# Performance work log

Measured on AMD Instinct MI355X. Metric: run time of the kernel, lower is better.

## Reference

```python
import jax, jax.numpy as jnp
import numpy as np
from jax import lax

BATCH, SEQ = 2, 2048
D_MODEL, D_STATE, D_CONV, D_INNER, DT_RANK = 1024, 16, 4, 2048, 64


def setup_inputs() -> dict:
    key = jax.random.key(0)
    ks = jax.random.split(key, 8)
    n = lambda k, shape, scale: (jax.random.normal(k, shape, jnp.float32) * scale)
    A = jnp.tile(jnp.arange(1, D_STATE + 1, dtype=jnp.float32), (D_INNER, 1))
    return {
        "hidden_states": n(ks[0], (BATCH, SEQ, D_MODEL), 1.0),
        "W_in": n(ks[1], (2 * D_INNER, D_MODEL), 0.02),
        "conv_w": n(ks[2], (D_INNER, 1, D_CONV), 0.3),
        "conv_b": n(ks[3], (D_INNER,), 0.02),
        "W_x": n(ks[4], (DT_RANK + 2 * D_STATE, D_INNER), 0.02),
        "W_dt": jax.random.uniform(ks[5], (D_INNER, DT_RANK), jnp.float32, -(DT_RANK ** -0.5), DT_RANK ** -0.5),
        "b_dt": n(ks[6], (D_INNER,), 0.02),
        "A_log": jnp.log(A),
        "D": jnp.ones((D_INNER,), jnp.float32),
        "W_out": n(ks[7], (D_MODEL, D_INNER), 0.02),
    }


def reference(hidden_states, W_in, conv_w, conv_b, W_x, W_dt, b_dt, A_log, D, W_out):
    # in_proj -> split into x and gate res
    xr = hidden_states @ W_in.T                      # (b, l, 2*d_inner)
    x, res = jnp.split(xr, 2, axis=-1)               # (b, l, d_inner) each

    # causal depthwise conv1d (torch pads both sides then truncates [:L] == left-pad d_conv-1)
    xc = lax.conv_general_dilated(
        x.transpose(0, 2, 1), conv_w, window_strides=(1,),
        padding=[(D_CONV - 1, 0)], feature_group_count=D_INNER)
    xc = xc + conv_b[None, :, None]
    u = jax.nn.silu(xc.transpose(0, 2, 1))           # (b, l, d_inner)

    # selective scan parameters (input-dependent)
    x_dbl = u @ W_x.T                                # (b, l, dt_rank + 2*d_state)
    dt = x_dbl[..., :DT_RANK]
    B = x_dbl[..., DT_RANK:DT_RANK + D_STATE]        # (b, l, n)
    C = x_dbl[..., DT_RANK + D_STATE:]               # (b, l, n)
    dt = jax.nn.softplus(dt @ W_dt.T + b_dt)         # (b, l, d_inner)

    A = -jnp.exp(A_log)                              # (d_inner, n)
    dA = jnp.exp(dt[..., None] * A)                  # (b, l, d, n)
    dBu = dt[..., None] * B[:, :, None, :] * u[..., None]  # (b, l, d, n)

    def step(h, inp):
        dA_t, dBu_t, C_t = inp                       # (b,d,n),(b,d,n),(b,n)
        h = dA_t * h + dBu_t
        return h, jnp.einsum('bdn,bn->bd', h, C_t)

    h0 = jnp.zeros((BATCH, D_INNER, D_STATE), u.dtype)
    _, ys = lax.scan(step, h0, (dA.transpose(1, 0, 2, 3),
                                dBu.transpose(1, 0, 2, 3),
                                C.transpose(1, 0, 2)))
    y = ys.transpose(1, 0, 2) + D * u                # (b, l, d_inner)

    y = y * jax.nn.silu(res)
    return y @ W_out.T                               # (b, l, d_model)
```

## Files before the change

### kernel.cpp

```cpp
#include <hip/hip_runtime.h>

typedef __bf16 bf16x8 __attribute__((ext_vector_type(8)));
typedef float f32x4 __attribute__((ext_vector_type(4)));
typedef unsigned short u16x8 __attribute__((ext_vector_type(8)));
typedef unsigned int u32;

#define SEQ_    2048
#define DM_     1024
#define DI_     2048
#define BATCH_  2
#define MTOT    4096
#define DSTATE  16
#define DTRANK  64
#define XDBLN   96
#define LCH     64
#define NCH     32

__device__ __forceinline__ float bf2f(unsigned short u){ return __uint_as_float(((unsigned)u) << 16); }
__device__ __forceinline__ unsigned short f2bf(float f){
  unsigned u = __float_as_uint(f);
  return (unsigned short)((u + 0x7fffu + ((u >> 16) & 1u)) >> 16);
}
__device__ __forceinline__ float silu_f(float v){ return v / (1.f + __expf(-v)); }
__device__ __forceinline__ float softplus_fast(float v){ return v > 20.f ? v : __logf(1.f + __expf(v)); }

__device__ __forceinline__ void load_lds16(const void* g, void* l){
  __builtin_amdgcn_global_load_lds((const __attribute__((address_space(1))) u32*)g,
                                   (__attribute__((address_space(3))) u32*)l, 16, 0, 0);
}

#define WAITV(n) do { asm volatile("s_waitcnt vmcnt(" #n ")" ::: "memory"); __builtin_amdgcn_sched_barrier(0); } while(0)
#define SBAR()   do { __builtin_amdgcn_s_barrier(); __builtin_amdgcn_sched_barrier(0); } while(0)

__global__ __launch_bounds__(256) void k_f2bf(const float* __restrict__ in, unsigned short* __restrict__ out, int n){
  int i = (blockIdx.x*256 + threadIdx.x)*4;
  if (i < n){
    float4 v = *(const float4*)(in + i);
    ushort4 o; o.x = f2bf(v.x); o.y = f2bf(v.y); o.z = f2bf(v.z); o.w = f2bf(v.w);
    *(ushort4*)(out + i) = o;
  }
}

__global__ __launch_bounds__(256) void k_wxpad(const float* __restrict__ wx, unsigned short* __restrict__ out){
  int i = (blockIdx.x*256 + threadIdx.x)*4;
  int row = i >> 11;
  ushort4 o;
  if (row < 96){
    float4 v = *(const float4*)(wx + i);
    o.x = f2bf(v.x); o.y = f2bf(v.y); o.z = f2bf(v.z); o.w = f2bf(v.w);
  } else { o.x = 0; o.y = 0; o.z = 0; o.w = 0; }
  *(ushort4*)(out + i) = o;
}

template<int NK>
__global__ __launch_bounds__(512, 1) void k_gemm8(const unsigned short* __restrict__ A,
                                                  const unsigned short* __restrict__ Bw,
                                                  unsigned short* __restrict__ oB0,
                                                  unsigned short* __restrict__ oB1)
{
  constexpr int K = NK*32;
  __shared__ unsigned short lds[65536];
  const int tid  = threadIdx.x;
  const int lane = tid & 63;
  const int wv = tid >> 6;
  const int wm = wv >> 2, wn = wv & 3;
  const int lr = lane & 15, lg = lane >> 4;
  const int prm = (lr >> 1) & 3;

  const unsigned short* Ab = A  + (size_t)blockIdx.y * 256 * K;
  const unsigned short* Bb = Bw + (size_t)blockIdx.x * 256 * K;

  const int r0 = tid >> 2;
  const int ch = tid & 3;

  auto issue = [&](int t){
    const int slot = (t & 3) * 8192;
    const int k0 = t * 32;
    #pragma unroll
    for (int c = 0; c < 2; ++c){
      int r = c*128 + r0;
      int e = slot + c*4096 + tid*8;
      int cl = k0 + ((ch ^ ((r >> 1) & 3)) << 3);
      load_lds16(Ab + (size_t)r*K + cl, &lds[e]);
      load_lds16(Bb + (size_t)r*K + cl, &lds[32768 + e]);
    }
  };

  f32x4 acc[8][4] = {};

  auto compute = [&](int t){
    const int slot = (t & 3) * 8192;
    bf16x8 af[8], bfr[4];
    #pragma unroll
    for (int mi = 0; mi < 8; ++mi)
      af[mi] = *(const bf16x8*)&lds[slot + (wm*128 + mi*16 + lr)*32 + ((lg ^ prm) << 3)];
    #pragma unroll
    for (int ni = 0; ni < 4; ++ni)
      bfr[ni] = *(const bf16x8*)&lds[32768 + slot + (wn*64 + ni*16 + lr)*32 + ((lg ^ prm) << 3)];
    __builtin_amdgcn_s_setprio(1);
    #pragma unroll
    for (int mi = 0; mi < 8; ++mi)
      #pragma unroll
      for (int ni = 0; ni < 4; ++ni)
        acc[mi][ni] = __builtin_amdgcn_mfma_f32_16x16x32_bf16(af[mi], bfr[ni], acc[mi][ni], 0, 0, 0);
    __builtin_amdgcn_s_setprio(0);
  };

  issue(0); issue(1); issue(2);
  WAITV(8); SBAR();

  for (int j = 0; j < NK-3; ++j){
    issue(j+3);
    compute(j);
    WAITV(8); SBAR();
  }
  compute(NK-3); WAITV(4); SBAR();
  compute(NK-2); WAITV(0); SBAR();
  compute(NK-1);

  const int rwv = blockIdx.y*256 + wm*128;
  const int cwv = blockIdx.x*256 + wn*64;
  #pragma unroll
  for (int mi = 0; mi < 8; ++mi)
    #pragma unroll
    for (int ni = 0; ni < 4; ++ni){
      int col = cwv + ni*16 + lr;
      #pragma unroll
      for (int rr = 0; rr < 4; ++rr){
        int row = rwv + mi*16 + lg*4 + rr;
        float v = acc[mi][ni][rr];
        if (col < DI_) oB0[(size_t)row*DI_ + col] = f2bf(v);
        else           oB1[(size_t)row*DI_ + (col - DI_)] = f2bf(silu_f(v));
      }
    }
}

__global__ __launch_bounds__(256) void k_gx(const unsigned short* __restrict__ A,
                                            const unsigned short* __restrict__ Bw,
                                            float* __restrict__ xdp)
{
  __shared__ unsigned short smraw[18432];
  unsigned short* lA0 = smraw;
  unsigned short* lB0 = smraw + 8192;
  const int tid = threadIdx.x;
  const int kz  = blockIdx.x;
  const unsigned short* Ab = A  + (size_t)blockIdx.y * 128 * 2048 + kz*512;
  const unsigned short* Bb = Bw + (size_t)kz*512;

  const int lane = tid & 63;
  const int wv = tid >> 6;
  const int wm = wv >> 1, wn = wv & 1;
  const int lr = lane & 15, lg = lane >> 4;

  f32x4 acc[4][4] = {};
  int cur = 0;
  const int e0 = tid*8;
  const int sl = tid & 3;
  #pragma unroll
  for (int c = 0; c < 2; ++c){
    int e = c*2048 + e0;
    int r = e >> 5;
    int cl = (sl ^ ((r >> 1) & 3)) << 3;
    load_lds16(Ab + (size_t)r*2048 + cl, lA0 + e);
    load_lds16(Bb + (size_t)r*2048 + cl, lB0 + e);
  }
  const int prm = (lr >> 1) & 3;
  for (int kt = 0; kt < 16; ++kt){
    __syncthreads();
    if (kt + 1 < 16){
      int k0 = (kt + 1) * 32;
      int nb = cur ^ 1;
      #pragma unroll
      for (int c = 0; c < 2; ++c){
        int e = c*2048 + e0;
        int r = e >> 5;
        int cl = (sl ^ ((r >> 1) & 3)) << 3;
        load_lds16(Ab + (size_t)r*2048 + k0 + cl, lA0 + nb*4096 + e);
        load_lds16(Bb + (size_t)r*2048 + k0 + cl, lB0 + nb*4096 + e);
      }
    }
    bf16x8 af[4], bfr[4];
    #pragma unroll
    for (int mi = 0; mi < 4; ++mi)
      af[mi] = *(const bf16x8*)&lA0[cur*4096 + (wm*64 + mi*16 + lr)*32 + (lg ^ prm)*8];
    #pragma unroll
    for (int ni = 0; ni < 4; ++ni)
      bfr[ni] = *(const bf16x8*)&lB0[cur*4096 + (wn*64 + ni*16 + lr)*32 + (lg ^ prm)*8];
    #pragma unroll
    for (int mi = 0; mi < 4; ++mi)
      #pragma unroll
      for (int ni = 0; ni < 4; ++ni)
        acc[mi][ni] = __builtin_amdgcn_mfma_f32_16x16x32_bf16(af[mi], bfr[ni], acc[mi][ni], 0, 0, 0);
    cur ^= 1;
  }

  __syncthreads();
  const int rw = blockIdx.y*128 + wm*64;
  const int cw = wn*64;
  float* outp = xdp + (size_t)kz*MTOT*128;
  float* st = (float*)smraw + wv*2304;
  #pragma unroll
  for (int h = 0; h < 2; ++h){
    #pragma unroll
    for (int mi = 0; mi < 4; ++mi)
      #pragma unroll
      for (int nn = 0; nn < 2; ++nn){
        int ni = h*2 + nn;
        #pragma unroll
        for (int r = 0; r < 4; ++r)
          st[(mi*16 + lg*4 + r)*36 + nn*16 + lr] = acc[mi][ni][r];
      }
    #pragma unroll
    for (int i = 0; i < 8; ++i){
      int lrow = i*8 + (lane >> 3);
      int col = cw + h*32 + (lane & 7)*4;
      float4 v = *(const float4*)&st[lrow*36 + (lane & 7)*4];
      *(float4*)(outp + (size_t)(rw + lrow)*128 + col) = v;
    }
  }
}

__global__ __launch_bounds__(256) void k_xfin(const float* __restrict__ xdp,
                                              float* __restrict__ xdbl,
                                              unsigned short* __restrict__ xdtb)
{
  int i = blockIdx.x*256 + threadIdx.x;
  int row = i / 24, j = i - row*24, c4 = j*4;
  const size_t o = (size_t)row*128 + c4;
  float4 s = *(const float4*)(xdp + o);
  #pragma unroll
  for (int p = 1; p < 4; ++p){
    float4 t = *(const float4*)(xdp + (size_t)p*(MTOT*128) + o);
    s.x += t.x; s.y += t.y; s.z += t.z; s.w += t.w;
  }
  if (c4 < 64){
    ushort4 ov; ov.x = f2bf(s.x); ov.y = f2bf(s.y); ov.z = f2bf(s.z); ov.w = f2bf(s.w);
    *(ushort4*)(xdtb + (size_t)row*64 + c4) = ov;
  } else {
    *(float4*)(xdbl + (size_t)row*XDBLN + c4) = s;
  }
}

__global__ __launch_bounds__(256) void k_gdt(const unsigned short* __restrict__ A,
                                             const unsigned short* __restrict__ Bw,
                                             float* __restrict__ oF,
                                             const float* __restrict__ bias)
{
  __shared__ unsigned short smraw[18432];
  unsigned short* lA0 = smraw;
  unsigned short* lB0 = smraw + 8192;
  const int tid = threadIdx.x;
  const unsigned short* Ab = A  + (size_t)blockIdx.y * 128 * 64;
  const unsigned short* Bb = Bw + (size_t)blockIdx.x * 128 * 64;

  const int lane = tid & 63;
  const int wv = tid >> 6;
  const int wm = wv >> 1, wn = wv & 1;
  const int lr = lane & 15, lg = lane >> 4;

  f32x4 acc[4][4] = {};
  int cur = 0;
  const int e0 = tid*8;
  const int sl = tid & 3;
  #pragma unroll
  for (int c = 0; c < 2; ++c){
    int e = c*2048 + e0;
    int r = e >> 5;
    int cl = (sl ^ ((r >> 1) & 3)) << 3;
    load_lds16(Ab + (size_t)r*64 + cl, lA0 + e);
    load_lds16(Bb + (size_t)r*64 + cl, lB0 + e);
  }
  const int prm = (lr >> 1) & 3;
  #pragma unroll
  for (int kt = 0; kt < 2; ++kt){
    __syncthreads();
    if (kt == 0){
      #pragma unroll
      for (int c = 0; c < 2; ++c){
        int e = c*2048 + e0;
        int r = e >> 5;
        int cl = (sl ^ ((r >> 1) & 3)) << 3;
        load_lds16(Ab + (size_t)r*64 + 32 + cl, lA0 + 4096 + e);
        load_lds16(Bb + (size_t)r*64 + 32 + cl, lB0 + 4096 + e);
      }
    }
    bf16x8 af[4], bfr[4];
    #pragma unroll
    for (int mi = 0; mi < 4; ++mi)
      af[mi] = *(const bf16x8*)&lA0[cur*4096 + (wm*64 + mi*16 + lr)*32 + (lg ^ prm)*8];
    #pragma unroll
    for (int ni = 0; ni < 4; ++ni)
      bfr[ni] = *(const bf16x8*)&lB0[cur*4096 + (wn*64 + ni*16 + lr)*32 + (lg ^ prm)*8];
    #pragma unroll
    for (int mi = 0; mi < 4; ++mi)
      #pragma unroll
      for (int ni = 0; ni < 4; ++ni)
        acc[mi][ni] = __builtin_amdgcn_mfma_f32_16x16x32_bf16(af[mi], bfr[ni], acc[mi][ni], 0, 0, 0);
    cur ^= 1;
  }

  __syncthreads();
  const int rw = blockIdx.y*128 + wm*64;
  const int cw = blockIdx.x*128 + wn*64;
  float* st = (float*)smraw + wv*2304;
  #pragma unroll
  for (int h = 0; h < 2; ++h){
    #pragma unroll
    for (int mi = 0; mi < 4; ++mi)
      #pragma unroll
      for (int nn = 0; nn < 2; ++nn){
        int ni = h*2 + nn;
        int col = cw + ni*16 + lr;
        #pragma unroll
        for (int r = 0; r < 4; ++r)
          st[(mi*16 + lg*4 + r)*36 + nn*16 + lr] = softplus_fast(acc[mi][ni][r] + bias[col]);
      }
    #pragma unroll
    for (int i = 0; i < 8; ++i){
      int lrow = i*8 + (lane >> 3);
      int col = cw + h*32 + (lane & 7)*4;
      float4 v = *(const float4*)&st[lrow*36 + (lane & 7)*4];
      *(float4*)(oF + (size_t)(rw + lrow)*DI_ + col) = v;
    }
  }
}

__global__ __launch_bounds__(256) void k_gout(const unsigned short* __restrict__ A,
                                              const unsigned short* __restrict__ Bw,
                                              float* __restrict__ oF)
{
  __shared__ unsigned short smraw[18432];
  unsigned short* lA0 = smraw;
  unsigned short* lB0 = smraw + 8192;
  const int tid = threadIdx.x;
  const unsigned short* Ab = A  + (size_t)blockIdx.y * 128 * 2048;
  const unsigned short* Bb = Bw + (size_t)blockIdx.x * 128 * 2048;

  const int lane = tid & 63;
  const int wv = tid >> 6;
  const int wm = wv >> 1, wn = wv & 1;
  const int lr = lane & 15, lg = lane >> 4;

  f32x4 acc[4][4] = {};
  int cur = 0;
  const int e0 = tid*8;
  const int sl = tid & 3;
  #pragma unroll
  for (int c = 0; c < 2; ++c){
    int e = c*2048 + e0;
    int r = e >> 5;
    int cl = (sl ^ ((r >> 1) & 3)) << 3;
    load_lds16(Ab + (size_t)r*2048 + cl, lA0 + e);
    load_lds16(Bb + (size_t)r*2048 + cl, lB0 + e);
  }
  const int prm = (lr >> 1) & 3;
  for (int kt = 0; kt < 64; ++kt){
    __syncthreads();
    if (kt + 1 < 64){
      int k0 = (kt + 1) * 32;
      int nb = cur ^ 1;
      #pragma unroll
      for (int c = 0; c < 2; ++c){
        int e = c*2048 + e0;
        int r = e >> 5;
        int cl = (sl ^ ((r >> 1) & 3)) << 3;
        load_lds16(Ab + (size_t)r*2048 + k0 + cl, lA0 + nb*4096 + e);
        load_lds16(Bb + (size_t)r*2048 + k0 + cl, lB0 + nb*4096 + e);
      }
    }
    bf16x8 af[4], bfr[4];
    #pragma unroll
    for (int mi = 0; mi < 4; ++mi)
      af[mi] = *(const bf16x8*)&lA0[cur*4096 + (wm*64 + mi*16 + lr)*32 + (lg ^ prm)*8];
    #pragma unroll
    for (int ni = 0; ni < 4; ++ni)
      bfr[ni] = *(const bf16x8*)&lB0[cur*4096 + (wn*64 + ni*16 + lr)*32 + (lg ^ prm)*8];
    #pragma unroll
    for (int mi = 0; mi < 4; ++mi)
      #pragma unroll
      for (int ni = 0; ni < 4; ++ni)
        acc[mi][ni] = __builtin_amdgcn_mfma_f32_16x16x32_bf16(af[mi], bfr[ni], acc[mi][ni], 0, 0, 0);
    cur ^= 1;
  }

  __syncthreads();
  const int rw = blockIdx.y*128 + wm*64;
  const int cw = blockIdx.x*128 + wn*64;
  float* st = (float*)smraw + wv*2304;
  #pragma unroll
  for (int h = 0; h < 2; ++h){
    #pragma unroll
    for (int mi = 0; mi < 4; ++mi)
      #pragma unroll
      for (int nn = 0; nn < 2; ++nn){
        int ni = h*2 + nn;
        #pragma unroll
        for (int r = 0; r < 4; ++r)
          st[(mi*16 + lg*4 + r)*36 + nn*16 + lr] = acc[mi][ni][r];
      }
    #pragma unroll
    for (int i = 0; i < 8; ++i){
      int lrow = i*8 + (lane >> 3);
      int col = cw + h*32 + (lane & 7)*4;
      float4 v = *(const float4*)&st[lrow*36 + (lane & 7)*4];
      *(float4*)(oF + (size_t)(rw + lrow)*DM_ + col) = v;
    }
  }
}

__global__ __launch_bounds__(256) void k_conv(const unsigned short* __restrict__ xb, const float* __restrict__ w,
                                              const float* __restrict__ cb, unsigned short* __restrict__ ub)
{
  const int d  = blockIdx.x*256 + threadIdx.x;
  const int t0 = blockIdx.y*64;
  const int b  = blockIdx.z;
  const float w0 = w[d*4+0], w1 = w[d*4+1], w2 = w[d*4+2], w3 = w[d*4+3], bias = cb[d];
  const size_t base = (size_t)(b*SEQ_)*DI_ + d;
  float xm3 = 0.f, xm2 = 0.f, xm1 = 0.f;
  if (t0 > 0){
    xm3 = bf2f(xb[base + (size_t)(t0-3)*DI_]);
    xm2 = bf2f(xb[base + (size_t)(t0-2)*DI_]);
    xm1 = bf2f(xb[base + (size_t)(t0-1)*DI_]);
  }
  for (int t = t0; t < t0 + 64; ++t){
    float xc = bf2f(xb[base + (size_t)t*DI_]);
    float acc = w0*xm3 + w1*xm2 + w2*xm1 + w3*xc + bias;
    ub[base + (size_t)t*DI_] = f2bf(silu_f(acc));
    xm3 = xm2; xm2 = xm1; xm1 = xc;
  }
}

__global__ __launch_bounds__(256) void k_scanA(const float* __restrict__ dtf, const unsigned short* __restrict__ ub,
                                               const float* __restrict__ xdbl, const float* __restrict__ alog,
                                               float* __restrict__ hloc, float* __restrict__ pprod)
{
  const int d = blockIdx.x*256 + threadIdx.x;
  const int c = blockIdx.y, b = blockIdx.z;
  __shared__ float sB[LCH][DSTATE];
  const size_t rowbase = (size_t)(b*SEQ_ + c*LCH);
  for (int i = threadIdx.x; i < LCH*DSTATE; i += 256){
    int t = i >> 4, n = i & 15;
    sB[t][n] = xdbl[(rowbase + t)*XDBLN + DTRANK + n];
  }
  __syncthreads();
  float a[16], h[16], p[16];
  #pragma unroll
  for (int n = 0; n < 16; ++n){
    a[n] = -__expf(alog[(size_t)d*16 + n]);
    h[n] = 0.f; p[n] = 1.f;
  }
  const size_t base = rowbase*DI_ + d;
  for (int t = 0; t < LCH; ++t){
    float dtv = dtf[base + (size_t)t*DI_];
    float uv  = bf2f(ub[base + (size_t)t*DI_]);
    float du  = dtv*uv;
    #pragma unroll
    for (int n = 0; n < 16; ++n){
      float da = __expf(dtv*a[n]);
      h[n] = da*h[n] + du*sB[t][n];
      p[n] *= da;
    }
  }
  const size_t o = ((size_t)(b*NCH + c)*DI_ + d)*16;
  #pragma unroll
  for (int n = 0; n < 16; ++n){ hloc[o+n] = h[n]; pprod[o+n] = p[n]; }
}

__global__ __launch_bounds__(256) void k_scanB(const float* __restrict__ hloc, const float* __restrict__ pprod,
                                               float* __restrict__ hinit)
{
  int i = blockIdx.x*256 + threadIdx.x;
  int b = i >> 15;
  int r = i & 32767;
  int d = r >> 4, n = r & 15;
  float H = 0.f;
  for (int c = 0; c < NCH; ++c){
    size_t o = ((size_t)(b*NCH + c)*DI_ + d)*16 + n;
    hinit[o] = H;
    H = pprod[o]*H + hloc[o];
  }
}

__global__ __launch_bounds__(256) void k_scanC(const float* __restrict__ dtf, const unsigned short* __restrict__ ub,
                                               const float* __restrict__ xdbl, const float* __restrict__ alog,
                                               const float* __restrict__ hinit, const float* __restrict__ Dvec,
                                               const unsigned short* __restrict__ sresb, unsigned short* __restrict__ yg)
{
  const int d = blockIdx.x*256 + threadIdx.x;
  const int c = blockIdx.y, b = blockIdx.z;
  __shared__ float sBC[LCH][32];
  const size_t rowbase = (size_t)(b*SEQ_ + c*LCH);
  for (int i = threadIdx.x; i < LCH*32; i += 256){
    int t = i >> 5, j = i & 31;
    sBC[t][j] = xdbl[(rowbase + t)*XDBLN + DTRANK + j];
  }
  __syncthreads();
  float a[16], h[16];
  const size_t o = ((size_t)(b*NCH + c)*DI_ + d)*16;
  #pragma unroll
  for (int n = 0; n < 16; ++n){
    a[n] = -__expf(alog[(size_t)d*16 + n]);
    h[n] = hinit[o + n];
  }
  const float Dd = Dvec[d];
  const size_t base = rowbase*DI_ + d;
  for (int t = 0; t < LCH; ++t){
    float dtv = dtf[base + (size_t)t*DI_];
    float uv  = bf2f(ub[base + (size_t)t*DI_]);
    float du  = dtv*uv;
    float y = 0.f;
    #pragma unroll
    for (int n = 0; n < 16; ++n){
      float da = __expf(dtv*a[n]);
      h[n] = da*h[n] + du*sBC[t][n];
      y += h[n]*sBC[t][16+n];
    }
    y += Dd*uv;
    float g = bf2f(sresb[base + (size_t)t*DI_]);
    yg[base + (size_t)t*DI_] = f2bf(y*g);
  }
}

extern "C" void kernel_launch(void* const* d_in, const int* in_sizes, int n_in,
                              void* d_out, int out_size, void* d_ws, size_t ws_size,
                              hipStream_t stream)
{
  const float* hs    = (const float*)d_in[0];
  const float* Win   = (const float*)d_in[1];
  const float* convw = (const float*)d_in[2];
  const float* convb = (const float*)d_in[3];
  const float* Wx    = (const float*)d_in[4];
  const float* Wdt   = (const float*)d_in[5];
  const float* bdt   = (const float*)d_in[6];
  const float* Alog  = (const float*)d_in[7];
  const float* Dvec  = (const float*)d_in[8];
  const float* Wout  = (const float*)d_in[9];
  float* out = (float*)d_out;

  char* p = (char*)d_ws;
  auto take = [&](size_t bytes) -> char* {
    char* r = p; p += (bytes + 255) & ~(size_t)255; return r;
  };
  unsigned short* hsb   = (unsigned short*)take((size_t)MTOT*DM_*2);
  unsigned short* winb  = (unsigned short*)take((size_t)2*DI_*DM_*2);
  unsigned short* woutb = (unsigned short*)take((size_t)DM_*DI_*2);
  unsigned short* wxpb  = (unsigned short*)take((size_t)128*DI_*2);
  unsigned short* wdtb  = (unsigned short*)take((size_t)DI_*DTRANK*2);
  unsigned short* xb    = (unsigned short*)take((size_t)MTOT*DI_*2);
  unsigned short* sresb = (unsigned short*)take((size_t)MTOT*DI_*2);
  unsigned short* ub    = (unsigned short*)take((size_t)MTOT*DI_*2);
  float*          xdp   = (float*)take((size_t)4*MTOT*128*4);
  float*          xdbl  = (float*)take((size_t)MTOT*XDBLN*4);
  unsigned short* xdtb  = (unsigned short*)take((size_t)MTOT*DTRANK*2);
  float*          dtf   = (float*)take((size_t)MTOT*DI_*4);
  float*          hloc  = (float*)take((size_t)BATCH_*NCH*DI_*16*4);
  float*          pprod = (float*)take((size_t)BATCH_*NCH*DI_*16*4);
  float*          hinit = (float*)take((size_t)BATCH_*NCH*DI_*16*4);
  unsigned short* yg    = (unsigned short*)take((size_t)MTOT*DI_*2);
  if ((size_t)(p - (char*)d_ws) > ws_size) return;

  k_f2bf <<<(MTOT*DM_/4 + 255)/256, 256, 0, stream>>>(hs,  hsb,  MTOT*DM_);
  k_f2bf <<<(2*DI_*DM_/4 + 255)/256, 256, 0, stream>>>(Win, winb, 2*DI_*DM_);
  k_f2bf <<<(DM_*DI_/4 + 255)/256, 256, 0, stream>>>(Wout, woutb, DM_*DI_);
  k_f2bf <<<(DI_*DTRANK/4 + 255)/256, 256, 0, stream>>>(Wdt, wdtb, DI_*DTRANK);
  k_wxpad<<<(128*DI_/4)/256, 256, 0, stream>>>(Wx, wxpb);

  k_gemm8<DM_/32><<<dim3(16, 16), 512, 0, stream>>>(hsb, winb, xb, sresb);

  k_conv<<<dim3(DI_/256, SEQ_/64, BATCH_), 256, 0, stream>>>(xb, convw, convb, ub);

  k_gx  <<<dim3(4, 32), 256, 0, stream>>>(ub, wxpb, xdp);
  k_xfin<<<(MTOT*24)/256, 256, 0, stream>>>(xdp, xdbl, xdtb);

  k_gdt<<<dim3(16, 32), 256, 0, stream>>>(xdtb, wdtb, dtf, bdt);

  k_scanA<<<dim3(DI_/256, NCH, BATCH_), 256, 0, stream>>>(dtf, ub, xdbl, Alog, hloc, pprod);
  k_scanB<<<(BATCH_*DI_*16)/256, 256, 0, stream>>>(hloc, pprod, hinit);
  k_scanC<<<dim3(DI_/256, NCH, BATCH_), 256, 0, stream>>>(dtf, ub, xdbl, Alog, hinit, Dvec, sresb, yg);

  k_gout<<<dim3(DM_/128, 32), 256, 0, stream>>>(yg, woutb, out);
}
```

Baseline: 242.0 us.

## Replace 256x256 in-proj GEMM with 128x128 tiles, remapped grid, staged stores

The in-projection GEMM moves from a 256x256-tile, 512-thread kernel with a 4-stage LDS pipeline to a 128x128-tile, 256-thread double-buffered kernel over 1024 blocks. Block indices are remapped so groups of 8 consecutive blocks share A/B panels, intended to improve cache (XCD/L2) locality, and the same remapping is applied to the output-projection GEMM. The epilogue now stages bf16 results through LDS for 16-byte coalesced stores instead of scattered 2-byte stores. The trade-off is more blocks and less data reuse per tile, and the simpler pipeline may hide memory latency less well.

Measured after the change: 250.9 us. 1.04x slower.

```diff
diff --git a/kernel.cpp b/kernel.cpp
--- a/kernel.cpp
+++ b/kernel.cpp
@@ -29,9 +29,6 @@
                                    (__attribute__((address_space(3))) u32*)l, 16, 0, 0);
 }
 
-#define WAITV(n) do { asm volatile("s_waitcnt vmcnt(" #n ")" ::: "memory"); __builtin_amdgcn_sched_barrier(0); } while(0)
-#define SBAR()   do { __builtin_amdgcn_s_barrier(); __builtin_amdgcn_sched_barrier(0); } while(0)
-
 __global__ __launch_bounds__(256) void k_f2bf(const float* __restrict__ in, unsigned short* __restrict__ out, int n){
   int i = (blockIdx.x*256 + threadIdx.x)*4;
   if (i < n){
@@ -52,87 +49,90 @@
   *(ushort4*)(out + i) = o;
 }
 
-template<int NK>
-__global__ __launch_bounds__(512, 1) void k_gemm8(const unsigned short* __restrict__ A,
-                                                  const unsigned short* __restrict__ Bw,
-                                                  unsigned short* __restrict__ oB0,
-                                                  unsigned short* __restrict__ oB1)
-{
-  constexpr int K = NK*32;
-  __shared__ unsigned short lds[65536];
-  const int tid  = threadIdx.x;
+__global__ __launch_bounds__(256) void k_gin(const unsigned short* __restrict__ A,
+                                             const unsigned short* __restrict__ Bw,
+                                             unsigned short* __restrict__ oX,
+                                             unsigned short* __restrict__ oR)
+{
+  __shared__ unsigned short smraw[20480];
+  unsigned short* lA0 = smraw;
+  unsigned short* lB0 = smraw + 8192;
+  const int tid = threadIdx.x;
+  const int bid = blockIdx.x;
+  const int k8 = bid & 7, cc = bid >> 3;
+  const int by = ((k8 & 1) << 4) + (cc >> 3);
+  const int bx = ((k8 >> 1) << 3) + (cc & 7);
+  const unsigned short* Ab = A  + (size_t)by * 128 * 1024;
+  const unsigned short* Bb = Bw + (size_t)bx * 128 * 1024;
+
   const int lane = tid & 63;
   const int wv = tid >> 6;
-  const int wm = wv >> 2, wn = wv & 3;
+  const int wm = wv >> 1, wn = wv & 1;
   const int lr = lane & 15, lg = lane >> 4;
+
+  f32x4 acc[4][4] = {};
+  int cur = 0;
+  const int e0 = tid*8;
+  const int sl = tid & 3;
+  #pragma unroll
+  for (int c = 0; c < 2; ++c){
+    int e = c*2048 + e0;
+    int r = e >> 5;
+    int cl = (sl ^ ((r >> 1) & 3)) << 3;
+    load_lds16(Ab + (size_t)r*1024 + cl, lA0 + e);
+    load_lds16(Bb + (size_t)r*1024 + cl, lB0 + e);
+  }
   const int prm = (lr >> 1) & 3;
-
-  const unsigned short* Ab = A  + (size_t)blockIdx.y * 256 * K;
-  const unsigned short* Bb = Bw + (size_t)blockIdx.x * 256 * K;
-
-  const int r0 = tid >> 2;
-  const int ch = tid & 3;
-
-  auto issue = [&](int t){
-    const int slot = (t & 3) * 8192;
-    const int k0 = t * 32;
-    #pragma unroll
-    for (int c = 0; c < 2; ++c){
-      int r = c*128 + r0;
-      int e = slot + c*4096 + tid*8;
-      int cl = k0 + ((ch ^ ((r >> 1) & 3)) << 3);
-      load_lds16(Ab + (size_t)r*K + cl, &lds[e]);
-      load_lds16(Bb + (size_t)r*K + cl, &lds[32768 + e]);
-    }
-  };
-
-  f32x4 acc[8][4] = {};
-
-  auto compute = [&](int t){
-    const int slot = (t & 3) * 8192;
-    bf16x8 af[8], bfr[4];
-    #pragma unroll
-    for (int mi = 0; mi < 8; ++mi)
-      af[mi] = *(const bf16x8*)&lds[slot + (wm*128 + mi*16 + lr)*32 + ((lg ^ prm) << 3)];
+  for (int kt = 0; kt < 32; ++kt){
+    __syncthreads();
+    if (kt + 1 < 32){
+      int k0 = (kt + 1) * 32;
+      int nb = cur ^ 1;
+      #pragma unroll
+      for (int c = 0; c < 2; ++c){
+        int e = c*2048 + e0;
+        int r = e >> 5;
+        int cl = (sl ^ ((r >> 1) & 3)) << 3;
+        load_lds16(Ab + (size_t)r*1024 + k0 + cl, lA0 + nb*4096 + e);
+        load_lds16(Bb + (size_t)r*1024 + k0 + cl, lB0 + nb*4096 + e);
+      }
+    }
+    bf16x8 af[4], bfr[4];
+    #pragma unroll
+    for (int mi = 0; mi < 4; ++mi)
+      af[mi] = *(const bf16x8*)&lA0[cur*4096 + (wm*64 + mi*16 + lr)*32 + (lg ^ prm)*8];
     #pragma unroll
     for (int ni = 0; ni < 4; ++ni)
-      bfr[ni] = *(const bf16x8*)&lds[32768 + slot + (wn*64 + ni*16 + lr)*32 + ((lg ^ prm) << 3)];
-    __builtin_amdgcn_s_setprio(1);
-    #pragma unroll
-    for (int mi = 0; mi < 8; ++mi)
+      bfr[ni] = *(const bf16x8*)&lB0[cur*4096 + (wn*64 + ni*16 + lr)*32 + (lg ^ prm)*8];
+    #pragma unroll
+    for (int mi = 0; mi < 4; ++mi)
       #pragma unroll
       for (int ni = 0; ni < 4; ++ni)
         acc[mi][ni] = __builtin_amdgcn_mfma_f32_16x16x32_bf16(af[mi], bfr[ni], acc[mi][ni], 0, 0, 0);
-    __builtin_amdgcn_s_setprio(0);
-  };
-
-  issue(0); issue(1); issue(2);
-  WAITV(8); SBAR();
-
-  for (int j = 0; j < NK-3; ++j){
-    issue(j+3);
-    compute(j);
-    WAITV(8); SBAR();
-  }
-  compute(NK-3); WAITV(4); SBAR();
-  compute(NK-2); WAITV(0); SBAR();
-  compute(NK-1);
-
-  const int rwv = blockIdx.y*256 + wm*128;
-  const int cwv = blockIdx.x*256 + wn*64;
-  #pragma unroll
-  for (int mi = 0; mi < 8; ++mi)
-    #pragma unroll
-    for (int ni = 0; ni < 4; ++ni){
-      int col = cwv + ni*16 + lr;
-      #pragma unroll
-      for (int rr = 0; rr < 4; ++rr){
-        int row = rwv + mi*16 + lg*4 + rr;
-        float v = acc[mi][ni][rr];
-        if (col < DI_) oB0[(size_t)row*DI_ + col] = f2bf(v);
-        else           oB1[(size_t)row*DI_ + (col - DI_)] = f2bf(silu_f(v));
-      }
-    }
+    cur ^= 1;
+  }
+
+  __syncthreads();
+  const bool hi = (bx >= 16);
+  const int rw  = by*128 + wm*64;
+  const int cwl = (hi ? bx - 16 : bx)*128 + wn*64;
+  unsigned short* st = smraw + wv*5120;
+  #pragma unroll
+  for (int mi = 0; mi < 4; ++mi)
+    #pragma unroll
+    for (int ni = 0; ni < 4; ++ni)
+      #pragma unroll
+      for (int r = 0; r < 4; ++r){
+        float v = acc[mi][ni][r];
+        st[(mi*16 + lg*4 + r)*80 + ni*16 + lr] = hi ? f2bf(silu_f(v)) : f2bf(v);
+      }
+  unsigned short* basep = (hi ? oR : oX) + (size_t)rw*DI_ + cwl;
+  #pragma unroll
+  for (int i = 0; i < 8; ++i){
+    int lrow = i*8 + (lane >> 3);
+    u16x8 v = *(const u16x8*)&st[lrow*80 + (lane & 7)*8];
+    *(u16x8*)(basep + (size_t)lrow*DI_ + (lane & 7)*8) = v;
+  }
 }
 
 __global__ __launch_bounds__(256) void k_gx(const unsigned short* __restrict__ A,
@@ -333,8 +333,12 @@
   unsigned short* lA0 = smraw;
   unsigned short* lB0 = smraw + 8192;
   const int tid = threadIdx.x;
-  const unsigned short* Ab = A  + (size_t)blockIdx.y * 128 * 2048;
-  const unsigned short* Bb = Bw + (size_t)blockIdx.x * 128 * 2048;
+  const int bid = blockIdx.x;
+  const int k8 = bid & 7, cc = bid >> 3;
+  const int by = k8*4 + (cc >> 3);
+  const int bx = cc & 7;
+  const unsigned short* Ab = A  + (size_t)by * 128 * 2048;
+  const unsigned short* Bb = Bw + (size_t)bx * 128 * 2048;
 
   const int lane = tid & 63;
   const int wv = tid >> 6;
@@ -384,8 +388,8 @@
   }
 
   __syncthreads();
-  const int rw = blockIdx.y*128 + wm*64;
-  const int cw = blockIdx.x*128 + wn*64;
+  const int rw = by*128 + wm*64;
+  const int cw = bx*128 + wn*64;
   float* st = (float*)smraw + wv*2304;
   #pragma unroll
   for (int h = 0; h < 2; ++h){
@@ -565,7 +569,7 @@
   k_f2bf <<<(DI_*DTRANK/4 + 255)/256, 256, 0, stream>>>(Wdt, wdtb, DI_*DTRANK);
   k_wxpad<<<(128*DI_/4)/256, 256, 0, stream>>>(Wx, wxpb);
 
-  k_gemm8<DM_/32><<<dim3(16, 16), 512, 0, stream>>>(hsb, winb, xb, sresb);
+  k_gin<<<1024, 256, 0, stream>>>(hsb, winb, xb, sresb);
 
   k_conv<<<dim3(DI_/256, SEQ_/64, BATCH_), 256, 0, stream>>>(xb, convw, convb, ub);
 
@@ -578,5 +582,5 @@
   k_scanB<<<(BATCH_*DI_*16)/256, 256, 0, stream>>>(hloc, pprod, hinit);
   k_scanC<<<dim3(DI_/256, NCH, BATCH_), 256, 0, stream>>>(dtf, ub, xdbl, Alog, hinit, Dvec, sresb, yg);
 
-  k_gout<<<dim3(DM_/128, 32), 256, 0, stream>>>(yg, woutb, out);
-}
+  k_gout<<<256, 256, 0, stream>>>(yg, woutb, out);
+}
```
